# Optimization experiments

Hardware: AMD Instinct MI355X
Metric: run time of the kernel (lower is better)

Reference implementation:

```python
import jax, jax.numpy as jnp
import numpy as np

B, T, V, E, H, K = 128, 512, 50257, 100, 128, 12
START, STOP = 10, 11


def setup_inputs() -> dict:
    key = jax.random.key(0)
    ks = jax.random.split(key, 11)
    sentences = jax.random.randint(ks[0], (B, T), 0, V)
    h0 = jax.random.normal(ks[1], (B, H), jnp.float32)
    c0 = jax.random.normal(ks[2], (B, H), jnp.float32)
    embed = jax.random.normal(ks[3], (V, E), jnp.float32) * 0.1
    Wih = jax.random.normal(ks[4], (4 * H, E), jnp.float32) * 0.1   # torch gate order i,f,g,o
    Whh = jax.random.normal(ks[5], (4 * H, H), jnp.float32) * 0.1
    bih = jax.random.normal(ks[6], (4 * H,), jnp.float32) * 0.1
    bhh = jax.random.normal(ks[7], (4 * H,), jnp.float32) * 0.1
    Wtag = jax.random.normal(ks[8], (K, H), jnp.float32) * 0.1
    btag = jax.random.normal(ks[9], (K,), jnp.float32) * 0.1
    transitions = jax.random.normal(ks[10], (K, K), jnp.float32)
    transitions = transitions.at[START, :].set(-10000.0).at[:, STOP].set(-10000.0)
    return dict(sentences=sentences, h0=h0, c0=c0, embed=embed,
                Wih=Wih, Whh=Whh, bih=bih, bhh=bhh,
                Wtag=Wtag, btag=btag, transitions=transitions)


def reference(sentences, h0, c0, embed, Wih, Whh, bih, bhh, Wtag, btag, transitions):
    # --- embedding + single-layer LSTM (batch_first); dropout is identity at eval ---
    x = embed[sentences]                       # [B, T, E]
    x_t = jnp.swapaxes(x, 0, 1)                # [T, B, E]

    def lstm_step(carry, xt):
        h, c = carry
        gates = xt @ Wih.T + h @ Whh.T + bih + bhh      # [B, 4H]
        i, f, g, o = jnp.split(gates, 4, axis=-1)
        c = jax.nn.sigmoid(f) * c + jax.nn.sigmoid(i) * jnp.tanh(g)
        h = jax.nn.sigmoid(o) * jnp.tanh(c)
        return (h, c), h

    _, hs = jax.lax.scan(lstm_step, (h0, c0), x_t)      # hs: [T, B, H]
    emissions = hs @ Wtag.T + btag                      # [T, B, K]

    # --- batched Viterbi DP over time ---
    def vit_step(prev, emit):
        # prev: [B, K] trellis at t-1; transitions[i, j] = score(i -> j)
        v = prev[:, :, None] + transitions[None]        # [B, K, K]
        best = jnp.max(v, axis=1)                       # [B, K]
        bp = jnp.argmax(v, axis=1).astype(jnp.int32)    # [B, K]
        return emit + best, bp

    last, bps = jax.lax.scan(vit_step, emissions[0], emissions[1:])  # bps: [T-1, B, K]
    scores = jnp.max(last, axis=-1)                     # [B]
    last_tag = jnp.argmax(last, axis=-1).astype(jnp.int32)  # [B]

    # --- backtrace (reverse scan) ---
    def back_step(tag, bp):
        prev = jnp.take_along_axis(bp, tag[:, None], axis=1)[:, 0]
        return prev, prev

    _, early_tags = jax.lax.scan(back_step, last_tag, bps, reverse=True)  # [T-1, B]
    paths = jnp.concatenate([early_tags, last_tag[None]], axis=0)         # [T, B]
    paths = jnp.swapaxes(paths, 0, 1)                                     # [B, T]
    return scores, paths
```

## Files before the change

### kernel.cpp

```cpp
#include <hip/hip_runtime.h>
#include <hip/hip_bf16.h>

#define BB 128
#define TT 512
#define EE 100
#define HH 128
#define KK 12
#define VV 50257
#define NB 8
#define NBLK 16
#define NPRE ((VV * 16 + 255) / 256)

typedef short bf16x8 __attribute__((ext_vector_type(8)));
typedef float f32x4  __attribute__((ext_vector_type(4)));

__device__ __forceinline__ unsigned short f2bf(float x) {
  __hip_bfloat16 h = __float2bfloat16(x);
  return *reinterpret_cast<unsigned short*>(&h);
}
__device__ __forceinline__ float bf2f(unsigned short u) {
  return __uint_as_float(((unsigned)u) << 16);
}

__device__ __forceinline__ bf16x8 load8_bf(const float* p) {
  float4 a = *reinterpret_cast<const float4*>(p);
  float4 b = *reinterpret_cast<const float4*>(p + 4);
  bf16x8 r;
  r[0] = (short)f2bf(a.x); r[1] = (short)f2bf(a.y);
  r[2] = (short)f2bf(a.z); r[3] = (short)f2bf(a.w);
  r[4] = (short)f2bf(b.x); r[5] = (short)f2bf(b.y);
  r[6] = (short)f2bf(b.z); r[7] = (short)f2bf(b.w);
  return r;
}

__device__ __forceinline__ bf16x8 load8_bf_pad_bias(const float* row, int k0,
                                                    float bias) {
  bf16x8 r;
  #pragma unroll
  for (int i = 0; i < 8; ++i) {
    int k = k0 + i;
    unsigned short v = 0;
    if (k < EE) v = f2bf(row[k]);
    else if (k == EE) v = f2bf(bias);
    r[i] = (short)v;
  }
  return r;
}

__device__ __forceinline__ int frag_idx(int b, int k) {
  return ((k >> 5) << 9) + ((b + (((k >> 3) & 3) << 4)) << 3) + (k & 7);
}

__device__ __forceinline__ void lds_barrier() {
  asm volatile("s_waitcnt lgkmcnt(0)\n\ts_barrier" ::: "memory");
}

__global__ __launch_bounds__(256) void prep_kernel(
    const float* __restrict__ embed, const float* __restrict__ Wih,
    const float* __restrict__ bih, const float* __restrict__ bhh,
    unsigned short* __restrict__ ebf, unsigned short* __restrict__ wbf)
{
  if (blockIdx.x < NPRE) {
    int id = blockIdx.x * 256 + threadIdx.x;
    if (id >= VV * 16) return;
    int v = id >> 4, g = id & 15;
    const float* row = embed + (size_t)v * EE;
    bf16x8 o;
    #pragma unroll
    for (int i = 0; i < 8; ++i) {
      int k = g * 8 + i;
      unsigned short u = 0;
      if (k < EE) u = f2bf(row[k]);
      else if (k == EE) u = 0x3F80;
      o[i] = (short)u;
    }
    *reinterpret_cast<bf16x8*>(ebf + (size_t)id * 8) = o;
  } else {
    int id = (blockIdx.x - NPRE) * 256 + threadIdx.x;
    if (id >= 8 * 4 * 4 * 64) return;
    int l = id & 63, kt = (id >> 6) & 3, tt = (id >> 8) & 3, s8 = id >> 10;
    int gcol = tt * HH + 16 * s8 + (l & 15);
    int k0 = kt * 32 + (l >> 4) * 8;
    float bias = bih[gcol] + bhh[gcol];
    bf16x8 r = load8_bf_pad_bias(Wih + (size_t)gcol * EE, k0, bias);
    *reinterpret_cast<bf16x8*>(wbf + (size_t)id * 8) = r;
  }
}

__global__ __launch_bounds__(256, 2) void pregates_kernel(
    const int* __restrict__ sent, const unsigned short* __restrict__ ebf,
    const unsigned short* __restrict__ wbf, unsigned short* __restrict__ P16)
{
  const int w = threadIdx.x >> 6, l = threadIdx.x & 63;
  const int c = l & 15, q = l >> 4;
  const int rt = blockIdx.x * 4 + w;
  const int flat = rt * 16 + c;
  const int b = flat >> 9, t = flat & 511;
  const int id = sent[b * TT + t];

  bf16x8 xa[4];
  #pragma unroll
  for (int kt = 0; kt < 4; ++kt)
    xa[kt] = *reinterpret_cast<const bf16x8*>(
        ebf + (size_t)id * 128 + kt * 32 + q * 8);

  const bf16x8* wb = reinterpret_cast<const bf16x8*>(wbf);
  #pragma unroll
  for (int s8 = 0; s8 < 8; ++s8) {
    f32x4 acc[4];
    #pragma unroll
    for (int tt = 0; tt < 4; ++tt) {
      f32x4 z = {0.f, 0.f, 0.f, 0.f};
      acc[tt] = z;
    }
    #pragma unroll
    for (int kt = 0; kt < 4; ++kt) {
      #pragma unroll
      for (int tt = 0; tt < 4; ++tt)
        acc[tt] = __builtin_amdgcn_mfma_f32_16x16x32_bf16(
            xa[kt], wb[((s8 * 4 + tt) * 4 + kt) * 64 + l], acc[tt], 0, 0, 0);
    }
    const int e = s8 * 16 + c;
    #pragma unroll
    for (int r4 = 0; r4 < 4; ++r4) {
      int fr = rt * 16 + q * 4 + r4;
      ushort4 o = make_ushort4(f2bf(acc[0][r4]), f2bf(acc[1][r4]),
                               f2bf(acc[2][r4]), f2bf(acc[3][r4]));
      *reinterpret_cast<ushort4*>(P16 + ((size_t)fr * 128 + e) * 4) = o;
    }
  }
}

__global__ __launch_bounds__(512, 2) void lstm_kernel(
    const unsigned short* __restrict__ P16, const float* __restrict__ Whh,
    const float* __restrict__ h0, const float* __restrict__ c0,
    unsigned short* __restrict__ hst)
{
  __shared__ __align__(16) unsigned short hfrag[2][2048];
  __shared__ __align__(16) unsigned int lpad[19456];

  const int bg  = blockIdx.x;
  const int tid = threadIdx.x;
  const int w   = tid >> 6;
  const int l   = tid & 63;
  const int c   = l & 15;
  const int q   = l >> 4;
  const int ew  = 16 * w + c;

  bf16x8 wh[4][4];
  #pragma unroll
  for (int tt = 0; tt < 4; ++tt) {
    const int gcol = tt * HH + ew;
    #pragma unroll
    for (int kt = 0; kt < 4; ++kt)
      wh[tt][kt] = load8_bf(Whh + (size_t)gcol * HH + kt * 32 + q * 8);
  }

  float cst[2];
  #pragma unroll
  for (int r = 0; r < 2; ++r)
    cst[r] = c0[(size_t)(bg * NB + q * 2 + r) * HH + ew];

  {
    int4 z = {0, 0, 0, 0};
    reinterpret_cast<int4*>(hfrag)[tid] = z;
  }
  for (int i = tid; i < 19456; i += 512) lpad[i] = 0u;
  unsigned int keep = lpad[tid];
  asm volatile("" :: "v"(keep));
  __syncthreads();

  for (int idx = tid; idx < NB * HH; idx += 512) {
    int lb = idx >> 7, k = idx & 127;
    int row = ((lb >> 1) << 2) + (lb & 1);
    hfrag[0][frag_idx(row, k)] = f2bf(h0[(size_t)(bg * NB + lb) * HH + k]);
  }

  const unsigned short* pb0 =
      P16 + (size_t)(bg * NB + q * 2 + 0) * (TT * 512) + ew * 4;
  const unsigned short* pb1 =
      P16 + (size_t)(bg * NB + q * 2 + 1) * (TT * 512) + ew * 4;
  ushort4 pA[2], pB[2];
  pA[0] = *reinterpret_cast<const ushort4*>(pb0);
  pA[1] = *reinterpret_cast<const ushort4*>(pb1);
  pB[0] = *reinterpret_cast<const ushort4*>(pb0 + 512);
  pB[1] = *reinterpret_cast<const ushort4*>(pb1 + 512);

  unsigned short hp[2] = {0, 0};
  unsigned short* hb0 = hst + (size_t)(bg * NB + q * 2 + 0) * TT * HH + ew;
  unsigned short* hb1 = hst + (size_t)(bg * NB + q * 2 + 1) * TT * HH + ew;

  const int hw_off = frag_idx(q * 4, ew);
  __syncthreads();

  auto step = [&](int s, ushort4 (&pcur)[2]) {
    const int rb = s & 1;

    if (s >= 1 && s <= TT) {
      hb0[(size_t)(s - 1) * HH] = hp[0];
      hb1[(size_t)(s - 1) * HH] = hp[1];
    }

    if (s < TT) {
      bf16x8 ha[4];
      const bf16x8* hr = reinterpret_cast<const bf16x8*>(&hfrag[rb][0]) + l;
      #pragma unroll
      for (int kt = 0; kt < 4; ++kt) ha[kt] = hr[kt * 64];

      f32x4 acc[4];
      #pragma unroll
      for (int tt = 0; tt < 4; ++tt) {
        f32x4 z = {0.f, 0.f, 0.f, 0.f};
        acc[tt] = z;
      }
      acc[0][0] = bf2f(pcur[0].x); acc[1][0] = bf2f(pcur[0].y);
      acc[2][0] = bf2f(pcur[0].z); acc[3][0] = bf2f(pcur[0].w);
      acc[0][1] = bf2f(pcur[1].x); acc[1][1] = bf2f(pcur[1].y);
      acc[2][1] = bf2f(pcur[1].z); acc[3][1] = bf2f(pcur[1].w);

      if (s + 2 < TT) {
        pcur[0] = *reinterpret_cast<const ushort4*>(pb0 + (size_t)(s + 2) * 512);
        pcur[1] = *reinterpret_cast<const ushort4*>(pb1 + (size_t)(s + 2) * 512);
      }

      #pragma unroll
      for (int kt = 0; kt < 4; ++kt) {
        #pragma unroll
        for (int tt = 0; tt < 4; ++tt)
          acc[tt] = __builtin_amdgcn_mfma_f32_16x16x32_bf16(ha[kt], wh[tt][kt], acc[tt], 0, 0, 0);
      }

      unsigned short* hwp = &hfrag[rb ^ 1][hw_off];
      #pragma unroll
      for (int r = 0; r < 2; ++r) {
        float ai  = __builtin_amdgcn_exp2f(acc[0][r] * -1.44269504f);
        float bgg = __builtin_amdgcn_exp2f(acc[2][r] * -2.88539008f);
        float af  = __builtin_amdgcn_exp2f(acc[1][r] * -1.44269504f);
        float ao  = __builtin_amdgcn_exp2f(acc[3][r] * -1.44269504f);
        float sitg = (1.0f - bgg) *
                     __builtin_amdgcn_rcpf((1.0f + ai) * (1.0f + bgg));
        float sf = __builtin_amdgcn_rcpf(1.0f + af);
        cst[r] = __fmaf_rn(sf, cst[r], sitg);
        float cc = __builtin_amdgcn_fmed3f(cst[r], -30.0f, 30.0f);
        float ec = __builtin_amdgcn_exp2f(cc * -2.88539008f);
        float hv = (1.0f - ec) *
                   __builtin_amdgcn_rcpf((1.0f + ao) * (1.0f + ec));
        unsigned short hu = f2bf(hv);
        hwp[r * 8] = hu;
        hp[r] = hu;
      }
    }
    lds_barrier();
  };

  for (int s = 0; s < TT + 2; s += 2) {
    step(s, pA);
    step(s + 1, pB);
  }
}

__global__ __launch_bounds__(64) void vit_kernel(
    const unsigned short* __restrict__ hst, const float* __restrict__ Wtag,
    const float* __restrict__ btag, const float* __restrict__ trans,
    float* __restrict__ out)
{
  __shared__ __align__(16) float trl[KK * 16];
  __shared__ __align__(16) float vbuf[16];
  __shared__ __align__(16) float ering[16 * 16];
  __shared__ unsigned char bp[TT * KK];
  __shared__ unsigned char path[TT];

  const int b = blockIdx.x, tid = threadIdx.x;
  const int c = tid & 15, q = tid >> 4;

  if (tid < KK * KK) {
    int i = tid / KK, jj = tid - i * KK;
    trl[jj * 16 + i] = trans[tid];
  }

  bf16x8 we[4];
  #pragma unroll
  for (int kt = 0; kt < 4; ++kt) {
    #pragma unroll
    for (int i = 0; i < 8; ++i) we[kt][i] = 0;
  }
  float bt = 0.f;
  if (c < KK) {
    #pragma unroll
    for (int kt = 0; kt < 4; ++kt)
      we[kt] = load8_bf(Wtag + (size_t)c * HH + kt * 32 + q * 8);
    bt = btag[c];
  }
  const unsigned short* hb = hst + (size_t)b * TT * HH;
  __syncthreads();

  for (int tb = 0; tb < TT; tb += 16) {
    bf16x8 ha[4];
    #pragma unroll
    for (int kt = 0; kt < 4; ++kt)
      ha[kt] = *reinterpret_cast<const bf16x8*>(
          hb + (size_t)(tb + c) * HH + kt * 32 + q * 8);
    f32x4 accE = {0.f, 0.f, 0.f, 0.f};
    #pragma unroll
    for (int kt = 0; kt < 4; ++kt)
      accE = __builtin_amdgcn_mfma_f32_16x16x32_bf16(ha[kt], we[kt], accE, 0, 0, 0);
    __syncthreads();
    #pragma unroll
    for (int r = 0; r < 4; ++r)
      ering[(q * 4 + r) * 16 + c] = accE[r] + bt;
    __syncthreads();

    #pragma unroll
    for (int i = 0; i < 16; ++i) {
      const int t = tb + i;
      if (tid < KK) {
        const int j = tid;
        float Ev = ering[i * 16 + j];
        float nv;
        if (t == 0) {
          nv = Ev;
        } else {
          float4 v0 = *reinterpret_cast<const float4*>(&vbuf[0]);
          float4 v1 = *reinterpret_cast<const float4*>(&vbuf[4]);
          float4 v2 = *reinterpret_cast<const float4*>(&vbuf[8]);
          float4 t0 = *reinterpret_cast<const float4*>(&trl[j * 16]);
          float4 t1 = *reinterpret_cast<const float4*>(&trl[j * 16 + 4]);
          float4 t2 = *reinterpret_cast<const float4*>(&trl[j * 16 + 8]);
          float cand[KK] = {v0.x + t0.x, v0.y + t0.y, v0.z + t0.z, v0.w + t0.w,
                            v1.x + t1.x, v1.y + t1.y, v1.z + t1.z, v1.w + t1.w,
                            v2.x + t2.x, v2.y + t2.y, v2.z + t2.z, v2.w + t2.w};
          float g0 = fmaxf(fmaxf(cand[0], cand[1]), cand[2]);
          float g1 = fmaxf(fmaxf(cand[3], cand[4]), cand[5]);
          float g2 = fmaxf(fmaxf(cand[6], cand[7]), cand[8]);
          float g3 = fmaxf(fmaxf(cand[9], cand[10]), cand[11]);
          float best = fmaxf(fmaxf(g0, g1), fmaxf(g2, g3));
          int bi = 11;
          #pragma unroll
          for (int k = 10; k >= 0; --k) bi = (cand[k] == best) ? k : bi;
          nv = Ev + best;
          bp[t * KK + j] = (unsigned char)bi;
        }
        vbuf[j] = nv;
      }
      __syncthreads();
    }
  }

  if (tid == 0) {
    float best = vbuf[0];
    int tag = 0;
    for (int jj = 1; jj < KK; ++jj)
      if (vbuf[jj] > best) { best = vbuf[jj]; tag = jj; }
    out[b] = best;
    path[TT - 1] = (unsigned char)tag;
    for (int t = TT - 1; t >= 1; --t) {
      tag = bp[t * KK + tag];
      path[t - 1] = (unsigned char)tag;
    }
  }
  __syncthreads();

  #pragma unroll
  for (int i = 0; i < 8; ++i)
    out[BB + (size_t)b * TT + tid + i * 64] = (float)path[tid + i * 64];
}

extern "C" void kernel_launch(void* const* d_in, const int* in_sizes, int n_in,
                              void* d_out, int out_size, void* d_ws, size_t ws_size,
                              hipStream_t stream) {
  const int*   sent  = (const int*)d_in[0];
  const float* h0    = (const float*)d_in[1];
  const float* c0    = (const float*)d_in[2];
  const float* embed = (const float*)d_in[3];
  const float* Wih   = (const float*)d_in[4];
  const float* Whh   = (const float*)d_in[5];
  const float* bih   = (const float*)d_in[6];
  const float* bhh   = (const float*)d_in[7];
  const float* Wtag  = (const float*)d_in[8];
  const float* btag  = (const float*)d_in[9];
  const float* trans = (const float*)d_in[10];
  float* out = (float*)d_out;

  unsigned short* ebf = (unsigned short*)d_ws;
  unsigned short* wbf = ebf + (size_t)VV * 128;
  unsigned short* P16 = wbf + 8192 * 8;
  unsigned short* hst = P16 + (size_t)BB * TT * 512;

  prep_kernel<<<NPRE + 32, 256, 0, stream>>>(embed, Wih, bih, bhh, ebf, wbf);
  pregates_kernel<<<(BB * TT / 16) / 4, 256, 0, stream>>>(sent, ebf, wbf, P16);
  lstm_kernel<<<NBLK, 512, 0, stream>>>(P16, Whh, h0, c0, hst);
  vit_kernel<<<BB, 64, 0, stream>>>(hst, Wtag, btag, trans, out);
}
```

Measured before the change: 530.8 us.

## Replace LDS barriers in Viterbi with wavefront shuffles and register state

The Viterbi kernel runs as a single 64-thread wavefront. This change holds the trellis values in registers and broadcasts them with __shfl instead of passing them through LDS with a __syncthreads per timestep. Transitions move into registers, the emission tile uses a double-buffered LDS ring, and the next h tile is prefetched. The serial single-thread backtrace becomes a wave-wide walk that loads backpointer words into registers and selects them by shuffle. This removes per-step barrier and LDS latency from the sequential DP, but depends on the block being exactly one wavefront and on the compiler ordering LDS accesses without explicit barriers.

New measurement: 515.8 us. 2.8% less time.

```diff
diff --git a/kernel.cpp b/kernel.cpp
--- a/kernel.cpp
+++ b/kernel.cpp
@@ -264,19 +264,18 @@
     const float* __restrict__ btag, const float* __restrict__ trans,
     float* __restrict__ out)
 {
-  __shared__ __align__(16) float trl[KK * 16];
-  __shared__ __align__(16) float vbuf[16];
-  __shared__ __align__(16) float ering[16 * 16];
+  __shared__ __align__(16) float ering[2][16 * 16];
   __shared__ unsigned char bp[TT * KK];
   __shared__ unsigned char path[TT];
 
   const int b = blockIdx.x, tid = threadIdx.x;
   const int c = tid & 15, q = tid >> 4;
-
-  if (tid < KK * KK) {
-    int i = tid / KK, jj = tid - i * KK;
-    trl[jj * 16 + i] = trans[tid];
-  }
+  const int j = tid;
+
+  float trl_r[KK];
+  #pragma unroll
+  for (int i = 0; i < KK; ++i)
+    trl_r[i] = (j < KK) ? trans[i * KK + j] : 0.f;
 
   bf16x8 we[4];
   #pragma unroll
@@ -292,73 +291,91 @@
     bt = btag[c];
   }
   const unsigned short* hb = hst + (size_t)b * TT * HH;
-  __syncthreads();
+
+  bf16x8 ha[4];
+  #pragma unroll
+  for (int kt = 0; kt < 4; ++kt)
+    ha[kt] = *reinterpret_cast<const bf16x8*>(
+        hb + (size_t)c * HH + kt * 32 + q * 8);
+
+  float v = 0.f;
 
   for (int tb = 0; tb < TT; tb += 16) {
-    bf16x8 ha[4];
-    #pragma unroll
-    for (int kt = 0; kt < 4; ++kt)
-      ha[kt] = *reinterpret_cast<const bf16x8*>(
-          hb + (size_t)(tb + c) * HH + kt * 32 + q * 8);
+    const int par = (tb >> 4) & 1;
+
     f32x4 accE = {0.f, 0.f, 0.f, 0.f};
     #pragma unroll
     for (int kt = 0; kt < 4; ++kt)
       accE = __builtin_amdgcn_mfma_f32_16x16x32_bf16(ha[kt], we[kt], accE, 0, 0, 0);
-    __syncthreads();
     #pragma unroll
     for (int r = 0; r < 4; ++r)
-      ering[(q * 4 + r) * 16 + c] = accE[r] + bt;
-    __syncthreads();
+      ering[par][(q * 4 + r) * 16 + c] = accE[r] + bt;
+
+    if (tb + 16 < TT) {
+      #pragma unroll
+      for (int kt = 0; kt < 4; ++kt)
+        ha[kt] = *reinterpret_cast<const bf16x8*>(
+            hb + (size_t)(tb + 16 + c) * HH + kt * 32 + q * 8);
+    }
+
+    float er[16];
+    #pragma unroll
+    for (int i = 0; i < 16; ++i) er[i] = ering[par][i * 16 + (j & 15)];
 
     #pragma unroll
     for (int i = 0; i < 16; ++i) {
       const int t = tb + i;
-      if (tid < KK) {
-        const int j = tid;
-        float Ev = ering[i * 16 + j];
-        float nv;
-        if (t == 0) {
-          nv = Ev;
-        } else {
-          float4 v0 = *reinterpret_cast<const float4*>(&vbuf[0]);
-          float4 v1 = *reinterpret_cast<const float4*>(&vbuf[4]);
-          float4 v2 = *reinterpret_cast<const float4*>(&vbuf[8]);
-          float4 t0 = *reinterpret_cast<const float4*>(&trl[j * 16]);
-          float4 t1 = *reinterpret_cast<const float4*>(&trl[j * 16 + 4]);
-          float4 t2 = *reinterpret_cast<const float4*>(&trl[j * 16 + 8]);
-          float cand[KK] = {v0.x + t0.x, v0.y + t0.y, v0.z + t0.z, v0.w + t0.w,
-                            v1.x + t1.x, v1.y + t1.y, v1.z + t1.z, v1.w + t1.w,
-                            v2.x + t2.x, v2.y + t2.y, v2.z + t2.z, v2.w + t2.w};
-          float g0 = fmaxf(fmaxf(cand[0], cand[1]), cand[2]);
-          float g1 = fmaxf(fmaxf(cand[3], cand[4]), cand[5]);
-          float g2 = fmaxf(fmaxf(cand[6], cand[7]), cand[8]);
-          float g3 = fmaxf(fmaxf(cand[9], cand[10]), cand[11]);
-          float best = fmaxf(fmaxf(g0, g1), fmaxf(g2, g3));
-          int bi = 11;
-          #pragma unroll
-          for (int k = 10; k >= 0; --k) bi = (cand[k] == best) ? k : bi;
-          nv = Ev + best;
-          bp[t * KK + j] = (unsigned char)bi;
-        }
-        vbuf[j] = nv;
-      }
-      __syncthreads();
-    }
-  }
-
+      float vv[KK];
+      #pragma unroll
+      for (int i2 = 0; i2 < KK; ++i2) vv[i2] = __shfl(v, i2);
+      if (t == 0) {
+        v = er[0];
+      } else {
+        float cand[KK];
+        #pragma unroll
+        for (int i2 = 0; i2 < KK; ++i2) cand[i2] = vv[i2] + trl_r[i2];
+        float g0 = fmaxf(fmaxf(cand[0], cand[1]), cand[2]);
+        float g1 = fmaxf(fmaxf(cand[3], cand[4]), cand[5]);
+        float g2 = fmaxf(fmaxf(cand[6], cand[7]), cand[8]);
+        float g3 = fmaxf(fmaxf(cand[9], cand[10]), cand[11]);
+        float best = fmaxf(fmaxf(g0, g1), fmaxf(g2, g3));
+        int bi = 11;
+        #pragma unroll
+        for (int k = 10; k >= 0; --k) bi = (cand[k] == best) ? k : bi;
+        v = er[i] + best;
+        if (j < KK) bp[t * KK + j] = (unsigned char)bi;
+      }
+    }
+  }
+
+  float vv[KK];
+  #pragma unroll
+  for (int i2 = 0; i2 < KK; ++i2) vv[i2] = __shfl(v, i2);
+  float best = vv[0];
+  int tag = 0;
+  #pragma unroll
+  for (int i2 = 1; i2 < KK; ++i2)
+    if (vv[i2] > best) { best = vv[i2]; tag = i2; }
   if (tid == 0) {
-    float best = vbuf[0];
-    int tag = 0;
-    for (int jj = 1; jj < KK; ++jj)
-      if (vbuf[jj] > best) { best = vbuf[jj]; tag = jj; }
     out[b] = best;
     path[TT - 1] = (unsigned char)tag;
-    for (int t = TT - 1; t >= 1; --t) {
-      tag = bp[t * KK + tag];
-      path[t - 1] = (unsigned char)tag;
-    }
-  }
-  __syncthreads();
+  }
+
+  for (int tb = TT - 64; tb >= 0; tb -= 64) {
+    const unsigned* bpw =
+        reinterpret_cast<const unsigned*>(bp + (size_t)(tb + tid) * KK);
+    unsigned r0 = bpw[0], r1 = bpw[1], r2 = bpw[2];
+    #pragma unroll
+    for (int i = 63; i >= 0; --i) {
+      const int t = tb + i;
+      if (t >= 1) {
+        unsigned d0 = __shfl(r0, i), d1 = __shfl(r1, i), d2 = __shfl(r2, i);
+        unsigned d = (tag < 4) ? d0 : ((tag < 8) ? d1 : d2);
+        tag = (int)((d >> ((tag & 3) * 8)) & 0xffu);
+        if (tid == 0) path[t - 1] = (unsigned char)tag;
+      }
+    }
+  }
 
   #pragma unroll
   for (int i = 0; i < 8; ++i)
```
